# Performance work log

Hardware: AMD Instinct MI355X
Metric: run time of the kernel (lower is better)

Reference implementation:

```python
import jax, jax.numpy as jnp
import numpy as np
import math

B, S, D_MODEL = 2, 8192, 1024
N_HEADS, HEAD_DIM = 16, 64
WINDOW = 512
SELECT_RATIO, MIN_SELECT, MAX_SELECT = 0.125, 16, 4096
CHUNK = 256
RMS_EPS = 1.1920929e-07  # torch.finfo(float32).eps (nn.RMSNorm default)
NEG_INF = -1e9


def _rope_cache(positions):
    # positions: [B, K] -> cos/sin [B, 1, K, HEAD_DIM//2]
    theta = 1.0 / (10000.0 ** (jnp.arange(0, HEAD_DIM, 2, dtype=jnp.float32) / HEAD_DIM))
    freqs = positions.astype(jnp.float32)[..., None] * theta  # [B,K,hD/2]
    return jnp.cos(freqs)[:, None], jnp.sin(freqs)[:, None]


def _apply_rope(x, cos_f, sin_f):
    # x: [B, nH, K, hD]
    x1, x2 = x[..., ::2], x[..., 1::2]
    return jnp.stack([x1 * cos_f - x2 * sin_f, x1 * sin_f + x2 * cos_f], axis=-1).reshape(x.shape)


def _routing_scores(x, cheby_out):
    abs_x = jnp.maximum(jnp.abs(x), 1e-7)
    x_ss = jnp.sign(x) * (1.0 - 1.0 / (1.0 + abs_x))
    error = x_ss[:, 1:, :] - cheby_out[:, :-1, :]
    scores = jnp.mean(jnp.abs(error), axis=-1)                    # [B, S-1]
    last = jnp.max(scores, axis=-1, keepdims=True)                # [B, 1]
    return jax.lax.stop_gradient(jnp.concatenate([scores, last], axis=-1))  # [B, S]


def _forward(x, cheby_out, W_qkv, W_o, rms_weight, diff_lambda_logit):
    K = min(max(MIN_SELECT, int(math.ceil(S * SELECT_RATIO))), S, MAX_SELECT)
    scores = _routing_scores(x, cheby_out)
    _, idx = jax.lax.top_k(scores, K)
    indices = jnp.sort(idx, axis=-1)                              # [B, K] sorted positions

    x_sel = jnp.take_along_axis(x, indices[:, :, None], axis=1)   # [B, K, D]
    qkv = x_sel @ W_qkv.T                                         # [B, K, 4D]
    q1, q2, k, v = jnp.split(qkv, 4, axis=-1)
    to_heads = lambda t: t.reshape(B, K, N_HEADS, HEAD_DIM).transpose(0, 2, 1, 3)
    q1, q2, k, v = to_heads(q1), to_heads(q2), to_heads(k), to_heads(v)

    cos_f, sin_f = _rope_cache(indices)
    q1 = _apply_rope(q1, cos_f, sin_f)
    q2 = _apply_rope(q2, cos_f, sin_f)
    k = _apply_rope(k, cos_f, sin_f)

    scale = 1.0 / math.sqrt(HEAD_DIM)
    outs1, outs2 = [], []
    for q_start in range(0, K, CHUNK):  # static loop over 4 chunks
        q_end = min(q_start + CHUNK, K)
        k_start = max(0, q_start - CHUNK)
        q1_c = q1[:, :, q_start:q_end]
        q2_c = q2[:, :, q_start:q_end]
        k_c = k[:, :, k_start:q_end]
        v_c = v[:, :, k_start:q_end]
        pos_q = indices[:, q_start:q_end].astype(jnp.float32)[:, :, None]  # [B,Cq,1]
        pos_k = indices[:, k_start:q_end].astype(jnp.float32)[:, None, :]  # [B,1,Ck]
        ok = (pos_k <= pos_q) & (pos_q - pos_k < WINDOW)
        bias = jnp.where(ok, 0.0, NEG_INF)[:, None]                # [B,1,Cq,Ck]
        s1 = jnp.einsum('bhqd,bhkd->bhqk', q1_c, k_c) * scale + bias
        s2 = jnp.einsum('bhqd,bhkd->bhqk', q2_c, k_c) * scale + bias
        outs1.append(jnp.einsum('bhqk,bhkd->bhqd', jax.nn.softmax(s1, axis=-1), v_c))
        outs2.append(jnp.einsum('bhqk,bhkd->bhqd', jax.nn.softmax(s2, axis=-1), v_c))
    out1 = jnp.concatenate(outs1, axis=2)
    out2 = jnp.concatenate(outs2, axis=2)

    lamb = jax.nn.sigmoid(diff_lambda_logit)[None, :, None, None]
    diff_out = (out1 - lamb * out2).transpose(0, 2, 1, 3).reshape(B, K, D_MODEL)

    output = jnp.zeros((B, S, D_MODEL), dtype=x.dtype)
    output = output.at[jnp.arange(B)[:, None], indices].set(diff_out)
    output = output @ W_o.T
    # RMSNorm
    var = jnp.mean(output * output, axis=-1, keepdims=True)
    output = output * jax.lax.rsqrt(var + RMS_EPS) * rms_weight
    return output


def setup_inputs() -> dict:
    key = jax.random.key(0)
    k0, k1, k2, k3 = jax.random.split(key, 4)
    return {
        'x': jax.random.normal(k0, (B, S, D_MODEL), jnp.float32),
        'cheby_out': jax.random.normal(k1, (B, S, D_MODEL), jnp.float32),
        'W_qkv': jax.random.normal(k2, (4 * D_MODEL, D_MODEL), jnp.float32) * 0.02,
        'W_o': jax.random.normal(k3, (D_MODEL, D_MODEL), jnp.float32) * 0.02,
        'rms_weight': jnp.ones((D_MODEL,), jnp.float32),
        'diff_lambda_logit': jnp.zeros((N_HEADS,), jnp.float32),
    }


def reference(x, cheby_out, W_qkv, W_o, rms_weight, diff_lambda_logit):
    return _forward(x, cheby_out, W_qkv, W_o, rms_weight, diff_lambda_logit)
```

## Files before the change

kernel.cpp:

```cpp
#include <hip/hip_runtime.h>
#include <math.h>

#define S_LEN   8192
#define DMODEL  1024
#define B_SZ    2
#define NH      16
#define HD      64
#define KSEL    1024
#define CHUNKQ  256
#define WINDOW  512
#define NEG_BIG -1000000000.0f
#define RMSEPS  1.1920929e-07f

typedef short bf16x8 __attribute__((ext_vector_type(8)));
typedef float f32x4 __attribute__((ext_vector_type(4)));

__global__ void k_zero(float4* __restrict__ o, int n4) {
    int i = blockIdx.x * blockDim.x + threadIdx.x;
    if (i < n4) o[i] = make_float4(0.f, 0.f, 0.f, 0.f);
}

__global__ __launch_bounds__(256) void k_scores(const float* __restrict__ x,
                                                const float* __restrict__ cheby,
                                                float* __restrict__ scores) {
    int lin = blockIdx.x;
    int b = lin / (S_LEN - 1);
    int t = lin % (S_LEN - 1);
    const float4* xr = (const float4*)(x + ((size_t)b * S_LEN + t + 1) * DMODEL);
    const float4* cr = (const float4*)(cheby + ((size_t)b * S_LEN + t) * DMODEL);
    float4 xv = xr[threadIdx.x];
    float4 cv = cr[threadIdx.x];
    double acc = 0.0;
    {
        float vs[4] = {xv.x, xv.y, xv.z, xv.w};
        float cs[4] = {cv.x, cv.y, cv.z, cv.w};
#pragma unroll
        for (int j = 0; j < 4; ++j) {
            float ax = fmaxf(fabsf(vs[j]), 1e-7f);
            float ss = copysignf(1.0f - 1.0f / (1.0f + ax), vs[j]);
            acc += (double)fabsf(ss - cs[j]);
        }
    }
    int lane = threadIdx.x & 63, wid = threadIdx.x >> 6;
#pragma unroll
    for (int o = 32; o; o >>= 1) acc += __shfl_down(acc, o);
    __shared__ double wred[4];
    if (lane == 0) wred[wid] = acc;
    __syncthreads();
    if (threadIdx.x == 0) {
        double tot = wred[0] + wred[1] + wred[2] + wred[3];
        scores[(size_t)b * S_LEN + t] = (float)(tot * (1.0 / 1024.0));
    }
}

__global__ __launch_bounds__(1024) void k_topk(const float* __restrict__ scores,
                                               int* __restrict__ indices) {
    const int b = blockIdx.x;
    const int tid = threadIdx.x;
    const int lane = tid & 63, wid = tid >> 6;
    __shared__ unsigned vals[S_LEN];
    __shared__ unsigned hist[256];
    __shared__ unsigned sfx[256];
    __shared__ unsigned wsum[16];
    __shared__ unsigned bcast[2];
    __shared__ float fred[16];

    float mx = -1e30f;
    for (int i = tid; i < S_LEN - 1; i += 1024) {
        float v = scores[(size_t)b * S_LEN + i];
        vals[i] = __float_as_uint(v);
        mx = fmaxf(mx, v);
    }
#pragma unroll
    for (int o = 32; o; o >>= 1) mx = fmaxf(mx, __shfl_down(mx, o));
    if (lane == 0) fred[wid] = mx;
    __syncthreads();
    if (tid == 0) {
        float m2 = fred[0];
        for (int w = 1; w < 16; ++w) m2 = fmaxf(m2, fred[w]);
        vals[S_LEN - 1] = __float_as_uint(m2);
    }
    __syncthreads();

    unsigned prefix = 0, remaining = KSEL;
    for (int p = 3; p >= 0; --p) {
        unsigned hm = (p == 3) ? 0u : (0xFFFFFFFFu << ((p + 1) * 8));
        if (tid < 256) hist[tid] = 0u;
        __syncthreads();
        for (int i = tid; i < S_LEN; i += 1024) {
            unsigned v = vals[i];
            if ((v & hm) == (prefix & hm))
                atomicAdd(&hist[(v >> (p * 8)) & 255u], 1u);
        }
        __syncthreads();
        if (tid < 256) sfx[tid] = hist[tid];
        __syncthreads();
        for (int off = 1; off < 256; off <<= 1) {
            unsigned add = 0;
            if (tid < 256 && tid + off < 256) add = sfx[tid + off];
            __syncthreads();
            if (tid < 256) sfx[tid] += add;
            __syncthreads();
        }
        if (tid < 256) {
            unsigned Sb  = sfx[tid];
            unsigned Sb1 = (tid < 255) ? sfx[tid + 1] : 0u;
            if (Sb >= remaining && Sb1 < remaining) { bcast[0] = (unsigned)tid; bcast[1] = Sb1; }
        }
        __syncthreads();
        prefix |= bcast[0] << (p * 8);
        remaining -= bcast[1];
        __syncthreads();
    }
    const unsigned T = prefix;
    const unsigned need = remaining;

    const int p0 = tid * 8;
    unsigned vloc[8];
#pragma unroll
    for (int j = 0; j < 8; ++j) vloc[j] = vals[p0 + j];

    unsigned eqpre[8]; unsigned myeq = 0;
#pragma unroll
    for (int j = 0; j < 8; ++j) { eqpre[j] = myeq; myeq += (vloc[j] == T) ? 1u : 0u; }
    unsigned inc = myeq;
#pragma unroll
    for (int o = 1; o < 64; o <<= 1) { unsigned u = __shfl_up(inc, o); if (lane >= o) inc += u; }
    if (lane == 63) wsum[wid] = inc;
    __syncthreads();
    if (wid == 0) {
        unsigned w = (lane < 16) ? wsum[lane] : 0u;
        unsigned winc = w;
#pragma unroll
        for (int o = 1; o < 16; o <<= 1) { unsigned u = __shfl_up(winc, o); if (lane >= o) winc += u; }
        if (lane < 16) wsum[lane] = winc - w;
    }
    __syncthreads();
    const unsigned eqbase = wsum[wid] + inc - myeq;
    __syncthreads();

    unsigned fpre[8]; unsigned myf = 0; unsigned fl = 0;
#pragma unroll
    for (int j = 0; j < 8; ++j) {
        bool f = (vloc[j] > T) || ((vloc[j] == T) && (eqbase + eqpre[j] < need));
        fl |= (f ? 1u : 0u) << j;
        fpre[j] = myf;
        myf += f ? 1u : 0u;
    }
    unsigned inc2 = myf;
#pragma unroll
    for (int o = 1; o < 64; o <<= 1) { unsigned u = __shfl_up(inc2, o); if (lane >= o) inc2 += u; }
    if (lane == 63) wsum[wid] = inc2;
    __syncthreads();
    if (wid == 0) {
        unsigned w = (lane < 16) ? wsum[lane] : 0u;
        unsigned winc = w;
#pragma unroll
        for (int o = 1; o < 16; o <<= 1) { unsigned u = __shfl_up(winc, o); if (lane >= o) winc += u; }
        if (lane < 16) wsum[lane] = winc - w;
    }
    __syncthreads();
    const unsigned fbase = wsum[wid] + inc2 - myf;
#pragma unroll
    for (int j = 0; j < 8; ++j)
        if ((fl >> j) & 1u)
            indices[b * KSEL + fbase + fpre[j]] = p0 + j;
}

__global__ void k_rope_tab(const int* __restrict__ idxs,
                           float* __restrict__ rcos, float* __restrict__ rsin) {
    int g = blockIdx.x * blockDim.x + threadIdx.x;
    if (g >= B_SZ * KSEL * 32) return;
    int i = g & 31, bm = g >> 5;
    int b = bm >> 10, m = bm & 1023;
    float pos = (float)idxs[b * KSEL + m];
    double th = exp2(-(double)i * (13.287712379549449 / 32.0));
    float freq = pos * (float)th;
    float s, c;
    sincosf(freq, &s, &c);
    rcos[g] = c;
    rsin[g] = s;
}

__global__ __launch_bounds__(256) void k_rope_apply(float* __restrict__ qkv,
                                                    const float* __restrict__ rcos,
                                                    const float* __restrict__ rsin) {
    int bm = blockIdx.x;
    float* row = qkv + (size_t)bm * 4096;
    for (int p = threadIdx.x; p < 1536; p += 256) {
        int s = p / 512, r = p % 512;
        int h = r >> 5, i = r & 31;
        float c = rcos[bm * 32 + i], sn = rsin[bm * 32 + i];
        int off = s * 1024 + h * 64 + 2 * i;
        float x1 = row[off], x2 = row[off + 1];
        row[off]     = x1 * c - x2 * sn;
        row[off + 1] = x1 * sn + x2 * c;
    }
}

__device__ __forceinline__ unsigned pack_hi2(float a, float b) {
    return (__float_as_uint(a) >> 16) | (__float_as_uint(b) & 0xFFFF0000u);
}
__device__ __forceinline__ unsigned pack_lo2(float a, float b) {
    unsigned ua = __float_as_uint(a), ub = __float_as_uint(b);
    float ra = a - __uint_as_float(ua & 0xFFFF0000u);
    float rb = b - __uint_as_float(ub & 0xFFFF0000u);
    unsigned la = __float_as_uint(ra), lb = __float_as_uint(rb);
    la = la + 0x7FFFu + ((la >> 16) & 1u);
    lb = lb + 0x7FFFu + ((lb >> 16) & 1u);
    return (la >> 16) | (lb & 0xFFFF0000u);
}
__device__ __forceinline__ uint4 pack_hi8(float4 a, float4 b) {
    return make_uint4(pack_hi2(a.x, a.y), pack_hi2(a.z, a.w),
                      pack_hi2(b.x, b.y), pack_hi2(b.z, b.w));
}
__device__ __forceinline__ uint4 pack_lo8(float4 a, float4 b) {
    return make_uint4(pack_lo2(a.x, a.y), pack_lo2(a.z, a.w),
                      pack_lo2(b.x, b.y), pack_lo2(b.z, b.w));
}

#define PADK 56

__global__ __launch_bounds__(256) void k_qkv(const float* __restrict__ x,
                                             const float* __restrict__ Wq,
                                             const int* __restrict__ idxs,
                                             float* __restrict__ qkv) {
    __shared__ ushort As[2][128][PADK];
    __shared__ ushort Bs[2][128][PADK];
    __shared__ int rows[128];
    const int tid = threadIdx.x;
    const int bm = blockIdx.x, bn = blockIdx.y;
    if (tid < 128) {
        int r = bm * 128 + tid;
        int bb = r >> 10, mm = r & 1023;
        rows[tid] = bb * S_LEN + idxs[bb * KSEL + mm];
    }
    __syncthreads();
    const int srow = tid >> 1, koff = (tid & 1) * 16;
    const float* asrc = x + (size_t)rows[srow] * DMODEL + koff;
    const float* bsrc = Wq + (size_t)(bn * 128 + srow) * DMODEL + koff;
    const int wave = tid >> 6, lane = tid & 63;
    const int wm = wave >> 1, wn = wave & 1;
    const int fr = lane & 15, fk = (lane >> 4) * 8;
    f32x4 acc[4][4];
#pragma unroll
    for (int i = 0; i < 4; ++i)
#pragma unroll
        for (int j = 0; j < 4; ++j) acc[i][j] = (f32x4){0.f, 0.f, 0.f, 0.f};
    float4 a_ld[4], b_ld[4];
#pragma unroll
    for (int i = 0; i < 4; ++i) {
        a_ld[i] = *(const float4*)(asrc + i * 4);
        b_ld[i] = *(const float4*)(bsrc + i * 4);
    }
    for (int k0 = 0; k0 < DMODEL; k0 += 32) {
        __syncthreads();
        *(uint4*)&As[0][srow][koff]     = pack_hi8(a_ld[0], a_ld[1]);
        *(uint4*)&As[0][srow][koff + 8] = pack_hi8(a_ld[2], a_ld[3]);
        *(uint4*)&As[1][srow][koff]     = pack_lo8(a_ld[0], a_ld[1]);
        *(uint4*)&As[1][srow][koff + 8] = pack_lo8(a_ld[2], a_ld[3]);
        *(uint4*)&Bs[0][srow][koff]     = pack_hi8(b_ld[0], b_ld[1]);
        *(uint4*)&Bs[0][srow][koff + 8] = pack_hi8(b_ld[2], b_ld[3]);
        *(uint4*)&Bs[1][srow][koff]     = pack_lo8(b_ld[0], b_ld[1]);
        *(uint4*)&Bs[1][srow][koff + 8] = pack_lo8(b_ld[2], b_ld[3]);
        __syncthreads();
        if (k0 + 32 < DMODEL) {
#pragma unroll
            for (int i = 0; i < 4; ++i) {
                a_ld[i] = *(const float4*)(asrc + k0 + 32 + i * 4);
                b_ld[i] = *(const float4*)(bsrc + k0 + 32 + i * 4);
            }
        }
        bf16x8 ah[4], al[4], bh[4], bl[4];
#pragma unroll
        for (int i = 0; i < 4; ++i) {
            ah[i] = *(const bf16x8*)&As[0][wm * 64 + i * 16 + fr][fk];
            al[i] = *(const bf16x8*)&As[1][wm * 64 + i * 16 + fr][fk];
            bh[i] = *(const bf16x8*)&Bs[0][wn * 64 + i * 16 + fr][fk];
            bl[i] = *(const bf16x8*)&Bs[1][wn * 64 + i * 16 + fr][fk];
        }
#pragma unroll
        for (int mi = 0; mi < 4; ++mi)
#pragma unroll
            for (int ni = 0; ni < 4; ++ni) {
                acc[mi][ni] = __builtin_amdgcn_mfma_f32_16x16x32_bf16(ah[mi], bh[ni], acc[mi][ni], 0, 0, 0);
                acc[mi][ni] = __builtin_amdgcn_mfma_f32_16x16x32_bf16(ah[mi], bl[ni], acc[mi][ni], 0, 0, 0);
                acc[mi][ni] = __builtin_amdgcn_mfma_f32_16x16x32_bf16(al[mi], bh[ni], acc[mi][ni], 0, 0, 0);
            }
    }
    const int r0 = (lane >> 4) * 4;
#pragma unroll
    for (int mi = 0; mi < 4; ++mi)
#pragma unroll
        for (int ni = 0; ni < 4; ++ni) {
#pragma unroll
            for (int r = 0; r < 4; ++r) {
                int row = bm * 128 + wm * 64 + mi * 16 + r0 + r;
                int col = bn * 128 + wn * 64 + ni * 16 + fr;
                qkv[(size_t)row * 4096 + col] = acc[mi][ni][r];
            }
        }
}

__global__ __launch_bounds__(256) void k_attn(const float* __restrict__ qkv,
                                              const int* __restrict__ idxs,
                                              float* __restrict__ o1,
                                              float* __restrict__ o2) {
    const int lin = blockIdx.x;
    const int qb = lin & 15;
    const int h  = (lin >> 4) & 15;
    const int b  = lin >> 8;
    const int tid = threadIdx.x;
    const int wave = tid >> 6, lane = tid & 63;
    const int qloc = lane >> 2, dp = lane & 3;
    const int qg = qb * 64 + wave * 16 + qloc;
    const int c = qg >> 8;
    const int cstart = (c >= 1) ? (c - 1) * 256 : 0;

    __shared__ float Kt[64][68];
    __shared__ float Vt[64][68];
    __shared__ int wred[4];

    const int* pidx = idxs + b * KSEL;
    const int pq = pidx[qg];
    int blo_ = cstart, bhi_ = qg;
    const int target = pq - WINDOW;
    while (blo_ < bhi_) {
        int mid = (blo_ + bhi_) >> 1;
        if (pidx[mid] > target) bhi_ = mid; else blo_ = mid + 1;
    }
    const int jlo = blo_;

    int wlo = jlo;
#pragma unroll
    for (int o = 32; o; o >>= 1) wlo = min(wlo, __shfl_xor(wlo, o));
    if (lane == 0) wred[wave] = wlo;
    __syncthreads();
    const int blo = min(min(wred[0], wred[1]), min(wred[2], wred[3]));
    const int t0 = blo >> 6;
    const int t1 = qb;

    const float* qrow = qkv + (size_t)(b * KSEL + qg) * 4096 + h * 64 + dp * 16;
    float4 q1v[4], q2v[4];
#pragma unroll
    for (int i = 0; i < 4; ++i) {
        q1v[i] = ((const float4*)qrow)[i];
        q2v[i] = ((const float4*)(qrow + 1024))[i];
    }
    float4 a1[4], a2[4];
#pragma unroll
    for (int i = 0; i < 4; ++i) {
        a1[i] = make_float4(0.f, 0.f, 0.f, 0.f);
        a2[i] = make_float4(0.f, 0.f, 0.f, 0.f);
    }
    float m1 = NEG_BIG, l1 = 0.f, m2 = NEG_BIG, l2 = 0.f;

    const float* kvsrc = qkv + (size_t)b * KSEL * 4096 + 2048 + h * 64;

    for (int t = t0; t <= t1; ++t) {
        __syncthreads();
        {
            const int kk = tid >> 2, cc = (tid & 3) * 16;
            const float* src = kvsrc + (size_t)(t * 64 + kk) * 4096 + cc;
#pragma unroll
            for (int i = 0; i < 4; ++i) {
                *(float4*)&Kt[kk][cc + 4 * i] = *(const float4*)(src + 4 * i);
                *(float4*)&Vt[kk][cc + 4 * i] = *(const float4*)(src + 1024 + 4 * i);
            }
        }
        __syncthreads();
        if (t * 64 + 63 >= wlo) {
#pragma unroll 4
            for (int j = 0; j < 64; ++j) {
                const int jg = t * 64 + j;
                const float* kr = &Kt[j][dp * 16];
                float4 k0 = *(const float4*)&kr[0];
                float4 k1 = *(const float4*)&kr[4];
                float4 k2 = *(const float4*)&kr[8];
                float4 k3 = *(const float4*)&kr[12];
                float p1a = q1v[0].x*k0.x + q1v[0].y*k0.y + q1v[0].z*k0.z + q1v[0].w*k0.w
                          + q1v[1].x*k1.x + q1v[1].y*k1.y + q1v[1].z*k1.z + q1v[1].w*k1.w
                          + q1v[2].x*k2.x + q1v[2].y*k2.y + q1v[2].z*k2.z + q1v[2].w*k2.w
                          + q1v[3].x*k3.x + q1v[3].y*k3.y + q1v[3].z*k3.z + q1v[3].w*k3.w;
                float p2a = q2v[0].x*k0.x + q2v[0].y*k0.y + q2v[0].z*k0.z + q2v[0].w*k0.w
                          + q2v[1].x*k1.x + q2v[1].y*k1.y + q2v[1].z*k1.z + q2v[1].w*k1.w
                          + q2v[2].x*k2.x + q2v[2].y*k2.y + q2v[2].z*k2.z + q2v[2].w*k2.w
                          + q2v[3].x*k3.x + q2v[3].y*k3.y + q2v[3].z*k3.z + q2v[3].w*k3.w;
                p1a += __shfl_xor(p1a, 1); p1a += __shfl_xor(p1a, 2);
                p2a += __shfl_xor(p2a, 1); p2a += __shfl_xor(p2a, 2);
                const bool ok = (jg >= jlo) && (jg <= qg);
                float sc1 = ok ? p1a * 0.125f : NEG_BIG;
                float sc2 = ok ? p2a * 0.125f : NEG_BIG;
                float d1 = sc1 - m1, d2 = sc2 - m2;
                if (__any(fmaxf(d1, d2) > 8.0f)) {
                    float nm1 = fmaxf(m1, sc1), nm2 = fmaxf(m2, sc2);
                    float sf1 = __expf(m1 - nm1), sf2 = __expf(m2 - nm2);
                    l1 *= sf1; l2 *= sf2;
#pragma unroll
                    for (int i = 0; i < 4; ++i) {
                        a1[i].x *= sf1; a1[i].y *= sf1; a1[i].z *= sf1; a1[i].w *= sf1;
                        a2[i].x *= sf2; a2[i].y *= sf2; a2[i].z *= sf2; a2[i].w *= sf2;
                    }
                    m1 = nm1; m2 = nm2;
                    d1 = sc1 - m1; d2 = sc2 - m2;
                }
                float p1 = __expf(d1), p2 = __expf(d2);
                l1 += p1; l2 += p2;
                const float* vr = &Vt[j][dp * 16];
                float4 v0 = *(const float4*)&vr[0];
                float4 v1 = *(const float4*)&vr[4];
                float4 v2 = *(const float4*)&vr[8];
                float4 v3 = *(const float4*)&vr[12];
                a1[0].x += p1*v0.x; a1[0].y += p1*v0.y; a1[0].z += p1*v0.z; a1[0].w += p1*v0.w;
                a1[1].x += p1*v1.x; a1[1].y += p1*v1.y; a1[1].z += p1*v1.z; a1[1].w += p1*v1.w;
                a1[2].x += p1*v2.x; a1[2].y += p1*v2.y; a1[2].z += p1*v2.z; a1[2].w += p1*v2.w;
                a1[3].x += p1*v3.x; a1[3].y += p1*v3.y; a1[3].z += p1*v3.z; a1[3].w += p1*v3.w;
                a2[0].x += p2*v0.x; a2[0].y += p2*v0.y; a2[0].z += p2*v0.z; a2[0].w += p2*v0.w;
                a2[1].x += p2*v1.x; a2[1].y += p2*v1.y; a2[1].z += p2*v1.z; a2[1].w += p2*v1.w;
                a2[2].x += p2*v2.x; a2[2].y += p2*v2.y; a2[2].z += p2*v2.z; a2[2].w += p2*v2.w;
                a2[3].x += p2*v3.x; a2[3].y += p2*v3.y; a2[3].z += p2*v3.z; a2[3].w += p2*v3.w;
            }
        }
    }
    const float i1 = 1.0f / l1, i2 = 1.0f / l2;
    const size_t obase = (size_t)(b * KSEL + qg) * 1024 + h * 64 + dp * 16;
    float* d1p = o1 + obase;
    float* d2p = o2 + obase;
#pragma unroll
    for (int i = 0; i < 4; ++i) {
        ((float4*)d1p)[i] = make_float4(a1[i].x * i1, a1[i].y * i1, a1[i].z * i1, a1[i].w * i1);
        ((float4*)d2p)[i] = make_float4(a2[i].x * i2, a2[i].y * i2, a2[i].z * i2, a2[i].w * i2);
    }
}

__global__ __launch_bounds__(256) void k_ogemm(const float* __restrict__ o1,
                                               const float* __restrict__ o2,
                                               const float* __restrict__ Wo,
                                               const float* __restrict__ dll,
                                               float* __restrict__ y) {
    __shared__ ushort As[2][128][PADK];
    __shared__ ushort Bs[2][64][PADK];
    __shared__ float lams[16];
    const int tid = threadIdx.x;
    const int bm = blockIdx.x, bn = blockIdx.y;
    if (tid < 16) lams[tid] = 1.0f / (1.0f + __expf(-dll[tid]));
    __syncthreads();
    const int srow = tid >> 1, koff = (tid & 1) * 16;
    const float* s1 = o1 + (size_t)(bm * 128 + srow) * 1024 + koff;
    const float* s2 = o2 + (size_t)(bm * 128 + srow) * 1024 + koff;
    const int browB = tid >> 2, koffB = (tid & 3) * 8;
    const float* bsrc = Wo + (size_t)(bn * 64 + browB) * 1024 + koffB;
    const int wave = tid >> 6, lane = tid & 63;
    const int wm = wave >> 1, wn = wave & 1;
    const int fr = lane & 15, fk = (lane >> 4) * 8;
    f32x4 acc[4][2];
#pragma unroll
    for (int i = 0; i < 4; ++i)
#pragma unroll
        for (int j = 0; j < 2; ++j) acc[i][j] = (f32x4){0.f, 0.f, 0.f, 0.f};
    float4 a1[4], a2[4], b_ld[2];
#pragma unroll
    for (int i = 0; i < 4; ++i) { a1[i] = *(const float4*)(s1 + i * 4); a2[i] = *(const float4*)(s2 + i * 4); }
    b_ld[0] = *(const float4*)(bsrc);
    b_ld[1] = *(const float4*)(bsrc + 4);
    for (int k0 = 0; k0 < 1024; k0 += 32) {
        float lam = lams[(k0 + koff) >> 6];
        float4 df[4];
#pragma unroll
        for (int i = 0; i < 4; ++i) {
            df[i].x = a1[i].x - lam * a2[i].x;
            df[i].y = a1[i].y - lam * a2[i].y;
            df[i].z = a1[i].z - lam * a2[i].z;
            df[i].w = a1[i].w - lam * a2[i].w;
        }
        __syncthreads();
        *(uint4*)&As[0][srow][koff]     = pack_hi8(df[0], df[1]);
        *(uint4*)&As[0][srow][koff + 8] = pack_hi8(df[2], df[3]);
        *(uint4*)&As[1][srow][koff]     = pack_lo8(df[0], df[1]);
        *(uint4*)&As[1][srow][koff + 8] = pack_lo8(df[2], df[3]);
        *(uint4*)&Bs[0][browB][koffB]   = pack_hi8(b_ld[0], b_ld[1]);
        *(uint4*)&Bs[1][browB][koffB]   = pack_lo8(b_ld[0], b_ld[1]);
        __syncthreads();
        if (k0 + 32 < 1024) {
#pragma unroll
            for (int i = 0; i < 4; ++i) {
                a1[i] = *(const float4*)(s1 + k0 + 32 + i * 4);
                a2[i] = *(const float4*)(s2 + k0 + 32 + i * 4);
            }
            b_ld[0] = *(const float4*)(bsrc + k0 + 32);
            b_ld[1] = *(const float4*)(bsrc + k0 + 36);
        }
        bf16x8 ah[4], al[4], bh[2], bl[2];
#pragma unroll
        for (int i = 0; i < 4; ++i) {
            ah[i] = *(const bf16x8*)&As[0][wm * 64 + i * 16 + fr][fk];
            al[i] = *(const bf16x8*)&As[1][wm * 64 + i * 16 + fr][fk];
        }
#pragma unroll
        for (int i = 0; i < 2; ++i) {
            bh[i] = *(const bf16x8*)&Bs[0][wn * 32 + i * 16 + fr][fk];
            bl[i] = *(const bf16x8*)&Bs[1][wn * 32 + i * 16 + fr][fk];
        }
#pragma unroll
        for (int mi = 0; mi < 4; ++mi)
#pragma unroll
            for (int ni = 0; ni < 2; ++ni) {
                acc[mi][ni] = __builtin_amdgcn_mfma_f32_16x16x32_bf16(ah[mi], bh[ni], acc[mi][ni], 0, 0, 0);
                acc[mi][ni] = __builtin_amdgcn_mfma_f32_16x16x32_bf16(ah[mi], bl[ni], acc[mi][ni], 0, 0, 0);
                acc[mi][ni] = __builtin_amdgcn_mfma_f32_16x16x32_bf16(al[mi], bh[ni], acc[mi][ni], 0, 0, 0);
            }
    }
    const int r0 = (lane >> 4) * 4;
#pragma unroll
    for (int mi = 0; mi < 4; ++mi)
#pragma unroll
        for (int ni = 0; ni < 2; ++ni) {
#pragma unroll
            for (int r = 0; r < 4; ++r) {
                int row = bm * 128 + wm * 64 + mi * 16 + r0 + r;
                int col = bn * 64 + wn * 32 + ni * 16 + fr;
                y[(size_t)row * 1024 + col] = acc[mi][ni][r];
            }
        }
}

__global__ __launch_bounds__(256) void k_rms(const float* __restrict__ y,
                                             const int* __restrict__ idxs,
                                             const float* __restrict__ w,
                                             float* __restrict__ out) {
    const int r = blockIdx.x;
    const int b = r >> 10, m = r & 1023;
    const float4 v = ((const float4*)(y + (size_t)r * 1024))[threadIdx.x];
    double ss = (double)v.x * v.x + (double)v.y * v.y + (double)v.z * v.z + (double)v.w * v.w;
    int lane = threadIdx.x & 63, wid = threadIdx.x >> 6;
#pragma unroll
    for (int o = 32; o; o >>= 1) ss += __shfl_down(ss, o);
    __shared__ double wr[4];
    if (lane == 0) wr[wid] = ss;
    __syncthreads();
    double tot = wr[0] + wr[1] + wr[2] + wr[3];
    float sc = 1.0f / sqrtf((float)(tot * (1.0 / 1024.0)) + RMSEPS);
    float4 wv = ((const float4*)w)[threadIdx.x];
    int row = idxs[b * KSEL + m];
    float4 o4 = make_float4((v.x * sc) * wv.x, (v.y * sc) * wv.y,
                            (v.z * sc) * wv.z, (v.w * sc) * wv.w);
    ((float4*)(out + ((size_t)b * S_LEN + row) * 1024))[threadIdx.x] = o4;
}

extern "C" void kernel_launch(void* const* d_in, const int* in_sizes, int n_in,
                              void* d_out, int out_size, void* d_ws, size_t ws_size,
                              hipStream_t stream) {
    (void)in_sizes; (void)n_in; (void)out_size; (void)ws_size;
    const float* x     = (const float*)d_in[0];
    const float* cheby = (const float*)d_in[1];
    const float* Wqkv  = (const float*)d_in[2];
    const float* Wo    = (const float*)d_in[3];
    const float* rmsw  = (const float*)d_in[4];
    const float* dll   = (const float*)d_in[5];
    float* out = (float*)d_out;

    float* ws = (float*)d_ws;
    float* scores = ws;
    int*   indices = (int*)(ws + 16384);
    float* rcos = ws + 16384 + 2048;
    float* rsin = rcos + 65536;
    float* qkv  = rsin + 65536;
    float* o1   = qkv + 8388608;
    float* o2   = o1 + 2097152;
    float* yb   = o2 + 2097152;

    k_zero<<<16384, 256, 0, stream>>>((float4*)out, (B_SZ * S_LEN * DMODEL) / 4);
    k_scores<<<B_SZ * (S_LEN - 1), 256, 0, stream>>>(x, cheby, scores);
    k_topk<<<B_SZ, 1024, 0, stream>>>(scores, indices);
    k_rope_tab<<<(B_SZ * KSEL * 32 + 255) / 256, 256, 0, stream>>>(indices, rcos, rsin);
    k_qkv<<<dim3(16, 32), 256, 0, stream>>>(x, Wqkv, indices, qkv);
    k_rope_apply<<<B_SZ * KSEL, 256, 0, stream>>>(qkv, rcos, rsin);
    k_attn<<<512, 256, 0, stream>>>(qkv, indices, o1, o2);
    k_ogemm<<<dim3(16, 16), 256, 0, stream>>>(o1, o2, Wo, dll, yb);
    k_rms<<<B_SZ * KSEL, 256, 0, stream>>>(yb, indices, rmsw, out);
}
```

Before: 393.5 us.

## Pre-split GEMM operands into bf16 hi/lo blocks and fuse diff into attention

Adds kernels that convert W_qkv, W_o and the gathered x rows into a blocked, pre-split bf16 hi/lo layout, so the GEMM main loops only copy ready bf16 data into XOR-swizzled shared memory. The per-tile float-to-bf16 split work and the padded LDS layout go away. The attention kernel now applies the lambda differential combine and writes the packed operand directly, which removes the separate o1/o2 fp32 buffers. The top-k histogram is made per-wave to reduce atomic contention. The cost is extra conversion launches and traffic for the weights on every call.

Result: slower. 544.2 us (+38.3%).

```diff
diff --git a/kernel.cpp b/kernel.cpp
--- a/kernel.cpp
+++ b/kernel.cpp
@@ -7,7 +7,6 @@
 #define NH      16
 #define HD      64
 #define KSEL    1024
-#define CHUNKQ  256
 #define WINDOW  512
 #define NEG_BIG -1000000000.0f
 #define RMSEPS  1.1920929e-07f
@@ -59,7 +58,7 @@
     const int tid = threadIdx.x;
     const int lane = tid & 63, wid = tid >> 6;
     __shared__ unsigned vals[S_LEN];
-    __shared__ unsigned hist[256];
+    __shared__ unsigned hist[16][256];
     __shared__ unsigned sfx[256];
     __shared__ unsigned wsum[16];
     __shared__ unsigned bcast[2];
@@ -85,15 +84,20 @@
     unsigned prefix = 0, remaining = KSEL;
     for (int p = 3; p >= 0; --p) {
         unsigned hm = (p == 3) ? 0u : (0xFFFFFFFFu << ((p + 1) * 8));
-        if (tid < 256) hist[tid] = 0u;
+        for (int i = tid; i < 4096; i += 1024) ((unsigned*)hist)[i] = 0u;
         __syncthreads();
         for (int i = tid; i < S_LEN; i += 1024) {
             unsigned v = vals[i];
             if ((v & hm) == (prefix & hm))
-                atomicAdd(&hist[(v >> (p * 8)) & 255u], 1u);
-        }
-        __syncthreads();
-        if (tid < 256) sfx[tid] = hist[tid];
+                atomicAdd(&hist[wid][(v >> (p * 8)) & 255u], 1u);
+        }
+        __syncthreads();
+        if (tid < 256) {
+            unsigned h = 0;
+#pragma unroll
+            for (int w = 0; w < 16; ++w) h += hist[w][tid];
+            sfx[tid] = h;
+        }
         __syncthreads();
         for (int off = 1; off < 256; off <<= 1) {
             unsigned add = 0;
@@ -219,65 +223,87 @@
                       pack_lo2(b.x, b.y), pack_lo2(b.z, b.w));
 }
 
-#define PADK 56
-
-__global__ __launch_bounds__(256) void k_qkv(const float* __restrict__ x,
-                                             const float* __restrict__ Wq,
-                                             const int* __restrict__ idxs,
+
+__global__ __launch_bounds__(256) void k_splitW(const float* __restrict__ src,
+                                                ushort* __restrict__ dst, int total) {
+    int idx = blockIdx.x * 256 + threadIdx.x;
+    int base = idx * 8;
+    if (base >= total) return;
+    int row = base >> 10, k = base & 1023;
+    int kblk = k >> 5, ko = k & 31;
+    float4 f0 = *(const float4*)(src + base);
+    float4 f1 = *(const float4*)(src + base + 4);
+    ushort* d = dst + ((size_t)row * 32 + kblk) * 64 + ko;
+    *(uint4*)d        = pack_hi8(f0, f1);
+    *(uint4*)(d + 32) = pack_lo8(f0, f1);
+}
+
+__global__ __launch_bounds__(256) void k_splitX(const float* __restrict__ x,
+                                                const int* __restrict__ idxs,
+                                                ushort* __restrict__ dst) {
+    const int r = blockIdx.x;
+    const int b = r >> 10, m = r & 1023;
+    const float* src = x + ((size_t)b * S_LEN + idxs[b * KSEL + m]) * DMODEL;
+    const int t = threadIdx.x;
+    const int k = t * 4;
+    float4 f = *(const float4*)(src + k);
+    int kblk = k >> 5, ko = k & 31;
+    ushort* d = dst + ((size_t)r * 32 + kblk) * 64 + ko;
+    uint2 hi = make_uint2(pack_hi2(f.x, f.y), pack_hi2(f.z, f.w));
+    uint2 lo = make_uint2(pack_lo2(f.x, f.y), pack_lo2(f.z, f.w));
+    *(uint2*)d        = hi;
+    *(uint2*)(d + 32) = lo;
+}
+
+__global__ __launch_bounds__(256) void k_qkv(const ushort* __restrict__ Xp,
+                                             const ushort* __restrict__ Wp,
                                              float* __restrict__ qkv) {
-    __shared__ ushort As[2][128][PADK];
-    __shared__ ushort Bs[2][128][PADK];
-    __shared__ int rows[128];
+    __shared__ ushort As[128][64];
+    __shared__ ushort Bs[128][64];
     const int tid = threadIdx.x;
     const int bm = blockIdx.x, bn = blockIdx.y;
-    if (tid < 128) {
-        int r = bm * 128 + tid;
-        int bb = r >> 10, mm = r & 1023;
-        rows[tid] = bb * S_LEN + idxs[bb * KSEL + mm];
-    }
-    __syncthreads();
-    const int srow = tid >> 1, koff = (tid & 1) * 16;
-    const float* asrc = x + (size_t)rows[srow] * DMODEL + koff;
-    const float* bsrc = Wq + (size_t)(bn * 128 + srow) * DMODEL + koff;
+    const int srow = tid >> 1, half = tid & 1;
+    const int r7 = srow & 7, c0 = half * 4;
+    const ushort* asrc = Xp + ((size_t)(bm * 128 + srow) * 32) * 64 + half * 32;
+    const ushort* bsrc = Wp + ((size_t)(bn * 128 + srow) * 32) * 64 + half * 32;
     const int wave = tid >> 6, lane = tid & 63;
     const int wm = wave >> 1, wn = wave & 1;
-    const int fr = lane & 15, fk = (lane >> 4) * 8;
+    const int fr = lane & 15, g = lane >> 4;
     f32x4 acc[4][4];
 #pragma unroll
     for (int i = 0; i < 4; ++i)
 #pragma unroll
         for (int j = 0; j < 4; ++j) acc[i][j] = (f32x4){0.f, 0.f, 0.f, 0.f};
-    float4 a_ld[4], b_ld[4];
+    uint4 av[4], bv[4];
 #pragma unroll
     for (int i = 0; i < 4; ++i) {
-        a_ld[i] = *(const float4*)(asrc + i * 4);
-        b_ld[i] = *(const float4*)(bsrc + i * 4);
-    }
-    for (int k0 = 0; k0 < DMODEL; k0 += 32) {
-        __syncthreads();
-        *(uint4*)&As[0][srow][koff]     = pack_hi8(a_ld[0], a_ld[1]);
-        *(uint4*)&As[0][srow][koff + 8] = pack_hi8(a_ld[2], a_ld[3]);
-        *(uint4*)&As[1][srow][koff]     = pack_lo8(a_ld[0], a_ld[1]);
-        *(uint4*)&As[1][srow][koff + 8] = pack_lo8(a_ld[2], a_ld[3]);
-        *(uint4*)&Bs[0][srow][koff]     = pack_hi8(b_ld[0], b_ld[1]);
-        *(uint4*)&Bs[0][srow][koff + 8] = pack_hi8(b_ld[2], b_ld[3]);
-        *(uint4*)&Bs[1][srow][koff]     = pack_lo8(b_ld[0], b_ld[1]);
-        *(uint4*)&Bs[1][srow][koff + 8] = pack_lo8(b_ld[2], b_ld[3]);
-        __syncthreads();
-        if (k0 + 32 < DMODEL) {
+        av[i] = ((const uint4*)asrc)[i];
+        bv[i] = ((const uint4*)bsrc)[i];
+    }
+    for (int kb = 0; kb < 32; ++kb) {
+        __syncthreads();
+#pragma unroll
+        for (int j = 0; j < 4; ++j) {
+            *(uint4*)&As[srow][((c0 + j) ^ r7) * 8] = av[j];
+            *(uint4*)&Bs[srow][((c0 + j) ^ r7) * 8] = bv[j];
+        }
+        __syncthreads();
+        if (kb + 1 < 32) {
 #pragma unroll
             for (int i = 0; i < 4; ++i) {
-                a_ld[i] = *(const float4*)(asrc + k0 + 32 + i * 4);
-                b_ld[i] = *(const float4*)(bsrc + k0 + 32 + i * 4);
+                av[i] = ((const uint4*)(asrc + (kb + 1) * 64))[i];
+                bv[i] = ((const uint4*)(bsrc + (kb + 1) * 64))[i];
             }
         }
         bf16x8 ah[4], al[4], bh[4], bl[4];
 #pragma unroll
         for (int i = 0; i < 4; ++i) {
-            ah[i] = *(const bf16x8*)&As[0][wm * 64 + i * 16 + fr][fk];
-            al[i] = *(const bf16x8*)&As[1][wm * 64 + i * 16 + fr][fk];
-            bh[i] = *(const bf16x8*)&Bs[0][wn * 64 + i * 16 + fr][fk];
-            bl[i] = *(const bf16x8*)&Bs[1][wn * 64 + i * 16 + fr][fk];
+            int ra = wm * 64 + i * 16 + fr;
+            int rb = wn * 64 + i * 16 + fr;
+            ah[i] = *(const bf16x8*)&As[ra][((g)     ^ (ra & 7)) * 8];
+            al[i] = *(const bf16x8*)&As[ra][((4 + g) ^ (ra & 7)) * 8];
+            bh[i] = *(const bf16x8*)&Bs[rb][((g)     ^ (rb & 7)) * 8];
+            bl[i] = *(const bf16x8*)&Bs[rb][((4 + g) ^ (rb & 7)) * 8];
         }
 #pragma unroll
         for (int mi = 0; mi < 4; ++mi)
@@ -288,7 +314,7 @@
                 acc[mi][ni] = __builtin_amdgcn_mfma_f32_16x16x32_bf16(al[mi], bh[ni], acc[mi][ni], 0, 0, 0);
             }
     }
-    const int r0 = (lane >> 4) * 4;
+    const int r0 = g * 4;
 #pragma unroll
     for (int mi = 0; mi < 4; ++mi)
 #pragma unroll
@@ -304,8 +330,8 @@
 
 __global__ __launch_bounds__(256) void k_attn(const float* __restrict__ qkv,
                                               const int* __restrict__ idxs,
-                                              float* __restrict__ o1,
-                                              float* __restrict__ o2) {
+                                              const float* __restrict__ dll,
+                                              ushort* __restrict__ Ap) {
     const int lin = blockIdx.x;
     const int qb = lin & 15;
     const int h  = (lin >> 4) & 15;
@@ -423,83 +449,81 @@
         }
     }
     const float i1 = 1.0f / l1, i2 = 1.0f / l2;
-    const size_t obase = (size_t)(b * KSEL + qg) * 1024 + h * 64 + dp * 16;
-    float* d1p = o1 + obase;
-    float* d2p = o2 + obase;
+    const float lam = 1.0f / (1.0f + __expf(-dll[h]));
+    float df[16];
 #pragma unroll
     for (int i = 0; i < 4; ++i) {
-        ((float4*)d1p)[i] = make_float4(a1[i].x * i1, a1[i].y * i1, a1[i].z * i1, a1[i].w * i1);
-        ((float4*)d2p)[i] = make_float4(a2[i].x * i2, a2[i].y * i2, a2[i].z * i2, a2[i].w * i2);
-    }
-}
-
-__global__ __launch_bounds__(256) void k_ogemm(const float* __restrict__ o1,
-                                               const float* __restrict__ o2,
-                                               const float* __restrict__ Wo,
-                                               const float* __restrict__ dll,
+        df[i*4+0] = a1[i].x * i1 - lam * (a2[i].x * i2);
+        df[i*4+1] = a1[i].y * i1 - lam * (a2[i].y * i2);
+        df[i*4+2] = a1[i].z * i1 - lam * (a2[i].z * i2);
+        df[i*4+3] = a1[i].w * i1 - lam * (a2[i].w * i2);
+    }
+    const int r = b * KSEL + qg;
+    const int kblk = h * 2 + (dp >> 1);
+    const int ko = (dp & 1) * 16;
+    ushort* d = Ap + ((size_t)r * 32 + kblk) * 64 + ko;
+    float4 f0 = make_float4(df[0], df[1], df[2], df[3]);
+    float4 f1 = make_float4(df[4], df[5], df[6], df[7]);
+    float4 f2 = make_float4(df[8], df[9], df[10], df[11]);
+    float4 f3 = make_float4(df[12], df[13], df[14], df[15]);
+    *(uint4*)(d)      = pack_hi8(f0, f1);
+    *(uint4*)(d + 8)  = pack_hi8(f2, f3);
+    *(uint4*)(d + 32) = pack_lo8(f0, f1);
+    *(uint4*)(d + 40) = pack_lo8(f2, f3);
+}
+
+__global__ __launch_bounds__(256) void k_ogemm(const ushort* __restrict__ Ap,
+                                               const ushort* __restrict__ Wp,
                                                float* __restrict__ y) {
-    __shared__ ushort As[2][128][PADK];
-    __shared__ ushort Bs[2][64][PADK];
-    __shared__ float lams[16];
+    __shared__ ushort As[128][64];
+    __shared__ ushort Bs[64][64];
     const int tid = threadIdx.x;
     const int bm = blockIdx.x, bn = blockIdx.y;
-    if (tid < 16) lams[tid] = 1.0f / (1.0f + __expf(-dll[tid]));
-    __syncthreads();
-    const int srow = tid >> 1, koff = (tid & 1) * 16;
-    const float* s1 = o1 + (size_t)(bm * 128 + srow) * 1024 + koff;
-    const float* s2 = o2 + (size_t)(bm * 128 + srow) * 1024 + koff;
-    const int browB = tid >> 2, koffB = (tid & 3) * 8;
-    const float* bsrc = Wo + (size_t)(bn * 64 + browB) * 1024 + koffB;
+    const int srow = tid >> 1, half = tid & 1;
+    const int ra7 = srow & 7, ca0 = half * 4;
+    const ushort* asrc = Ap + ((size_t)(bm * 128 + srow) * 32) * 64 + half * 32;
+    const int brow = tid >> 2, q = tid & 3;
+    const int rb7 = brow & 7;
+    const ushort* bsrc = Wp + ((size_t)(bn * 64 + brow) * 32) * 64 + q * 16;
     const int wave = tid >> 6, lane = tid & 63;
     const int wm = wave >> 1, wn = wave & 1;
-    const int fr = lane & 15, fk = (lane >> 4) * 8;
+    const int fr = lane & 15, g = lane >> 4;
     f32x4 acc[4][2];
 #pragma unroll
     for (int i = 0; i < 4; ++i)
 #pragma unroll
         for (int j = 0; j < 2; ++j) acc[i][j] = (f32x4){0.f, 0.f, 0.f, 0.f};
-    float4 a1[4], a2[4], b_ld[2];
-#pragma unroll
-    for (int i = 0; i < 4; ++i) { a1[i] = *(const float4*)(s1 + i * 4); a2[i] = *(const float4*)(s2 + i * 4); }
-    b_ld[0] = *(const float4*)(bsrc);
-    b_ld[1] = *(const float4*)(bsrc + 4);
-    for (int k0 = 0; k0 < 1024; k0 += 32) {
-        float lam = lams[(k0 + koff) >> 6];
-        float4 df[4];
+    uint4 av[4], bv[2];
+#pragma unroll
+    for (int i = 0; i < 4; ++i) av[i] = ((const uint4*)asrc)[i];
+    bv[0] = ((const uint4*)bsrc)[0];
+    bv[1] = ((const uint4*)bsrc)[1];
+    for (int kb = 0; kb < 32; ++kb) {
+        __syncthreads();
+#pragma unroll
+        for (int j = 0; j < 4; ++j)
+            *(uint4*)&As[srow][((ca0 + j) ^ ra7) * 8] = av[j];
+        *(uint4*)&Bs[brow][((q * 2)     ^ rb7) * 8] = bv[0];
+        *(uint4*)&Bs[brow][((q * 2 + 1) ^ rb7) * 8] = bv[1];
+        __syncthreads();
+        if (kb + 1 < 32) {
+#pragma unroll
+            for (int i = 0; i < 4; ++i) av[i] = ((const uint4*)(asrc + (kb + 1) * 64))[i];
+            bv[0] = ((const uint4*)(bsrc + (kb + 1) * 64))[0];
+            bv[1] = ((const uint4*)(bsrc + (kb + 1) * 64))[1];
+        }
+        bf16x8 ah[4], al[4], bh[2], bl[2];
 #pragma unroll
         for (int i = 0; i < 4; ++i) {
-            df[i].x = a1[i].x - lam * a2[i].x;
-            df[i].y = a1[i].y - lam * a2[i].y;
-            df[i].z = a1[i].z - lam * a2[i].z;
-            df[i].w = a1[i].w - lam * a2[i].w;
-        }
-        __syncthreads();
-        *(uint4*)&As[0][srow][koff]     = pack_hi8(df[0], df[1]);
-        *(uint4*)&As[0][srow][koff + 8] = pack_hi8(df[2], df[3]);
-        *(uint4*)&As[1][srow][koff]     = pack_lo8(df[0], df[1]);
-        *(uint4*)&As[1][srow][koff + 8] = pack_lo8(df[2], df[3]);
-        *(uint4*)&Bs[0][browB][koffB]   = pack_hi8(b_ld[0], b_ld[1]);
-        *(uint4*)&Bs[1][browB][koffB]   = pack_lo8(b_ld[0], b_ld[1]);
-        __syncthreads();
-        if (k0 + 32 < 1024) {
-#pragma unroll
-            for (int i = 0; i < 4; ++i) {
-                a1[i] = *(const float4*)(s1 + k0 + 32 + i * 4);
-                a2[i] = *(const float4*)(s2 + k0 + 32 + i * 4);
-            }
-            b_ld[0] = *(const float4*)(bsrc + k0 + 32);
-            b_ld[1] = *(const float4*)(bsrc + k0 + 36);
-        }
-        bf16x8 ah[4], al[4], bh[2], bl[2];
-#pragma unroll
-        for (int i = 0; i < 4; ++i) {
-            ah[i] = *(const bf16x8*)&As[0][wm * 64 + i * 16 + fr][fk];
-            al[i] = *(const bf16x8*)&As[1][wm * 64 + i * 16 + fr][fk];
+            int ra = wm * 64 + i * 16 + fr;
+            ah[i] = *(const bf16x8*)&As[ra][((g)     ^ (ra & 7)) * 8];
+            al[i] = *(const bf16x8*)&As[ra][((4 + g) ^ (ra & 7)) * 8];
         }
 #pragma unroll
         for (int i = 0; i < 2; ++i) {
-            bh[i] = *(const bf16x8*)&Bs[0][wn * 32 + i * 16 + fr][fk];
-            bl[i] = *(const bf16x8*)&Bs[1][wn * 32 + i * 16 + fr][fk];
+            int rb = wn * 32 + i * 16 + fr;
+            bh[i] = *(const bf16x8*)&Bs[rb][((g)     ^ (rb & 7)) * 8];
+            bl[i] = *(const bf16x8*)&Bs[rb][((4 + g) ^ (rb & 7)) * 8];
         }
 #pragma unroll
         for (int mi = 0; mi < 4; ++mi)
@@ -510,7 +534,7 @@
                 acc[mi][ni] = __builtin_amdgcn_mfma_f32_16x16x32_bf16(al[mi], bh[ni], acc[mi][ni], 0, 0, 0);
             }
     }
-    const int r0 = (lane >> 4) * 4;
+    const int r0 = g * 4;
 #pragma unroll
     for (int mi = 0; mi < 4; ++mi)
 #pragma unroll
@@ -562,20 +586,24 @@
     float* ws = (float*)d_ws;
     float* scores = ws;
     int*   indices = (int*)(ws + 16384);
-    float* rcos = ws + 16384 + 2048;
+    float* rcos = ws + 18432;
     float* rsin = rcos + 65536;
     float* qkv  = rsin + 65536;
-    float* o1   = qkv + 8388608;
-    float* o2   = o1 + 2097152;
-    float* yb   = o2 + 2097152;
+    ushort* XpAp = (ushort*)(qkv + 8388608);
+    ushort* Wqp  = (ushort*)((float*)XpAp + 2097152);
+    ushort* Wop  = (ushort*)((float*)Wqp + 4194304);
+    float* yb    = (float*)Wop + 1048576;
 
     k_zero<<<16384, 256, 0, stream>>>((float4*)out, (B_SZ * S_LEN * DMODEL) / 4);
     k_scores<<<B_SZ * (S_LEN - 1), 256, 0, stream>>>(x, cheby, scores);
+    k_splitW<<<2048, 256, 0, stream>>>(Wqkv, Wqp, 4096 * 1024);
+    k_splitW<<<512, 256, 0, stream>>>(Wo, Wop, 1024 * 1024);
     k_topk<<<B_SZ, 1024, 0, stream>>>(scores, indices);
     k_rope_tab<<<(B_SZ * KSEL * 32 + 255) / 256, 256, 0, stream>>>(indices, rcos, rsin);
-    k_qkv<<<dim3(16, 32), 256, 0, stream>>>(x, Wqkv, indices, qkv);
+    k_splitX<<<B_SZ * KSEL, 256, 0, stream>>>(x, indices, XpAp);
+    k_qkv<<<dim3(16, 32), 256, 0, stream>>>(XpAp, Wqp, qkv);
     k_rope_apply<<<B_SZ * KSEL, 256, 0, stream>>>(qkv, rcos, rsin);
-    k_attn<<<512, 256, 0, stream>>>(qkv, indices, o1, o2);
-    k_ogemm<<<dim3(16, 16), 256, 0, stream>>>(o1, o2, Wo, dll, yb);
+    k_attn<<<512, 256, 0, stream>>>(qkv, indices, dll, XpAp);
+    k_ogemm<<<dim3(16, 16), 256, 0, stream>>>(XpAp, Wop, yb);
     k_rms<<<B_SZ * KSEL, 256, 0, stream>>>(yb, indices, rmsw, out);
 }
```
